# Performance work log

Hardware: AMD Instinct MI355X
Metric: run time of the kernel (lower is better)

Reference implementation:

```python
import jax, jax.numpy as jnp
import numpy as np

HEADS = 4

def setup_inputs() -> dict:
    B, L, D = 4, 2048, 256
    key = jax.random.key(0)
    k1, k2, k3, k4, k5, k6 = jax.random.split(key, 6)
    return {
        "atten": jax.random.normal(k1, (B, L, L), dtype=jnp.float32),
        "value": jax.random.normal(k2, (B, L, D), dtype=jnp.float32),
        "mask": jax.random.uniform(k3, (B, 1, L, L), dtype=jnp.float32),
        "padding_mask": jax.random.randint(k4, (B, L, L), 0, 2, dtype=jnp.int32),
        "Wv": jax.random.normal(k5, (D, D), dtype=jnp.float32) * 0.02,
        "bv": jnp.zeros((D,), dtype=jnp.float32),
        "Wo": jax.random.normal(k6, (D, D), dtype=jnp.float32) * 0.02,
        "bo": jnp.zeros((D,), dtype=jnp.float32),
    }

def reference(atten, value, mask, padding_mask, Wv, bv, Wo, bo):
    B, L, D = value.shape
    H = HEADS
    dk = D // H
    # to_value: Linear then split heads. N == 1 (value.unsqueeze(1) in torch).
    v = value @ Wv + bv                                   # (B, L, D)
    v = v.reshape(B, 1, L, H, dk).transpose(0, 3, 1, 2, 4)  # (B, H, N=1, L, dk)
    # externally supplied attention logits, two sequential masked fills
    a = atten[:, None, :, :]                              # (B, 1, L, L)
    a = jnp.where(mask < 0.5, jnp.finfo(a.dtype).min, a)
    a = jnp.where(padding_mask[:, None, :, :] == 0, -jnp.inf, a)
    a = jax.nn.softmax(a, axis=-1)                        # (B, 1, L, L)
    # dropout is identity in eval mode
    # einsum 'bhij,bhnjk->bhnik' with h=1 on a broadcast across H heads of v
    out = jnp.einsum('bij,bhnjk->bhnik', a[:, 0], v)      # (B, H, 1, L, dk)
    out = out.transpose(0, 2, 3, 1, 4).reshape(B, 1, L, D)
    out = out @ Wo + bo                                   # (B, 1, L, D)
    return out
```

## Files before the change

### kernel.cpp

```cpp
#include <hip/hip_runtime.h>
#include <hip/hip_bf16.h>
#include <math.h>

#define L 2048
#define D 256

typedef __attribute__((ext_vector_type(8))) short bf16x8;
typedef __attribute__((ext_vector_type(4))) float f32x4;
typedef __attribute__((ext_vector_type(4))) int i32x4;

__device__ __forceinline__ unsigned short f2bf(float f) {
    union { float f; unsigned int u; } v; v.f = f;
    unsigned int r = v.u + 0x7FFFu + ((v.u >> 16) & 1u);
    return (unsigned short)(r >> 16);
}

__global__ __launch_bounds__(256) void wtrans_kernel(
    const float* __restrict__ Wv, const float* __restrict__ Wo,
    unsigned short* __restrict__ Wvt, unsigned short* __restrict__ Wot) {
    int idx = blockIdx.x * 256 + threadIdx.x;
    int which = idx >> 16;
    int e = idx & 65535;
    int n = e >> 8, k = e & 255;
    const float* W = which ? Wo : Wv;
    unsigned short* Wt = which ? Wot : Wvt;
    Wt[n * 256 + k] = f2bf(W[k * 256 + n]);
}

__global__ __launch_bounds__(256) void gemm_v_kernel(
    const float* __restrict__ A,
    const unsigned short* __restrict__ Wt,
    const float* __restrict__ bias,
    unsigned short* __restrict__ Vt) {
    const int wave = threadIdx.x >> 6;
    const int lane = threadIdx.x & 63;
    const int mh = wave >> 1, nh = wave & 1;
    const int lm = lane & 15, q = lane >> 4;
    const int m0 = blockIdx.x * 64;
    const int n0 = blockIdx.y * 128;

    f32x4 acc[2][4];
#pragma unroll
    for (int i = 0; i < 2; i++)
#pragma unroll
        for (int j = 0; j < 4; j++) acc[i][j] = (f32x4)(0.f);

    int arow[2];
    arow[0] = m0 + mh * 32 + lm;
    arow[1] = arow[0] + 16;
    int ncol[4];
#pragma unroll
    for (int nf = 0; nf < 4; nf++) ncol[nf] = n0 + nh * 64 + nf * 16 + lm;

    for (int k0 = 0; k0 < 256; k0 += 32) {
        int kq = k0 + q * 8;
        bf16x8 bfr[4];
#pragma unroll
        for (int nf = 0; nf < 4; nf++)
            bfr[nf] = *reinterpret_cast<const bf16x8*>(Wt + ncol[nf] * 256 + kq);
        bf16x8 afr[2];
#pragma unroll
        for (int mf = 0; mf < 2; mf++) {
            const float* ap = A + arow[mf] * 256 + kq;
            f32x4 a0 = *reinterpret_cast<const f32x4*>(ap);
            f32x4 a1 = *reinterpret_cast<const f32x4*>(ap + 4);
            bf16x8 t;
#pragma unroll
            for (int e = 0; e < 4; e++) t[e] = (short)f2bf(a0[e]);
#pragma unroll
            for (int e = 0; e < 4; e++) t[4 + e] = (short)f2bf(a1[e]);
            afr[mf] = t;
        }
#pragma unroll
        for (int mf = 0; mf < 2; mf++)
#pragma unroll
            for (int nf = 0; nf < 4; nf++)
                acc[mf][nf] = __builtin_amdgcn_mfma_f32_16x16x32_bf16(
                    afr[mf], bfr[nf], acc[mf][nf], 0, 0, 0);
    }

#pragma unroll
    for (int mf = 0; mf < 2; mf++) {
        int mrow = m0 + mh * 32 + mf * 16 + q * 4;
#pragma unroll
        for (int nf = 0; nf < 4; nf++) {
            int n = ncol[nf];
            float bias_n = bias[n];
            int b = mrow >> 11;
            int j = mrow & 2047;
            unsigned short* dst = Vt + (size_t)b * (D * L) + (size_t)n * L + j;
            ushort4 pk;
            pk.x = f2bf(acc[mf][nf][0] + bias_n);
            pk.y = f2bf(acc[mf][nf][1] + bias_n);
            pk.z = f2bf(acc[mf][nf][2] + bias_n);
            pk.w = f2bf(acc[mf][nf][3] + bias_n);
            *reinterpret_cast<ushort4*>(dst) = pk;
        }
    }
}

__global__ __launch_bounds__(256) void p_kernel(
    const float* __restrict__ atten, const float* __restrict__ mask,
    const int* __restrict__ pad, unsigned short* __restrict__ P,
    float* __restrict__ lsum2) {
    const int wid = blockIdx.x * 4 + (threadIdx.x >> 6);
    const int row = wid >> 1, h = wid & 1;
    const int lane = threadIdx.x & 63;

    const size_t base = (size_t)row * L + h * 1024 + lane * 4;
    const float* at = atten + base;
    const float* mk = mask  + base;
    const int*   pd = pad   + base;
    unsigned short* Pr = P + base;

    f32x4 a0 = *reinterpret_cast<const f32x4*>(at);
    f32x4 m0 = *reinterpret_cast<const f32x4*>(mk);
    i32x4 p0 = *reinterpret_cast<const i32x4*>(pd);

    float l_th = 0.f;
#pragma unroll
    for (int c = 0; c < 4; c++) {
        f32x4 a1, m1; i32x4 p1;
        if (c < 3) {
            const int off = (c + 1) * 256;
            a1 = *reinterpret_cast<const f32x4*>(at + off);
            m1 = *reinterpret_cast<const f32x4*>(mk + off);
            p1 = *reinterpret_cast<const i32x4*>(pd + off);
        }
        ushort4 pk;
        float pv;
        pv = (m0[0] < 0.5f || p0[0] == 0) ? 0.f : __expf(a0[0]); l_th += pv; pk.x = f2bf(pv);
        pv = (m0[1] < 0.5f || p0[1] == 0) ? 0.f : __expf(a0[1]); l_th += pv; pk.y = f2bf(pv);
        pv = (m0[2] < 0.5f || p0[2] == 0) ? 0.f : __expf(a0[2]); l_th += pv; pk.z = f2bf(pv);
        pv = (m0[3] < 0.5f || p0[3] == 0) ? 0.f : __expf(a0[3]); l_th += pv; pk.w = f2bf(pv);
        *reinterpret_cast<ushort4*>(Pr + c * 256) = pk;
        a0 = a1; m0 = m1; p0 = p1;
    }
#pragma unroll
    for (int off = 1; off < 64; off <<= 1) l_th += __shfl_xor(l_th, off);
    if (lane == 0) lsum2[wid] = l_th;
}

__global__ __launch_bounds__(256) void pv_split_kernel(
    const unsigned short* __restrict__ P, const unsigned short* __restrict__ Vt,
    float* __restrict__ part) {
    const int rb = blockIdx.x;
    const int sk = blockIdx.y;
    const int tid = threadIdx.x;
    const int w = tid >> 6, lane = tid & 63;
    const int lm = lane & 15, q = lane >> 4;
    const int b = rb >> 6;
    const int row0 = rb * 32;

    const unsigned short* pA = P + (size_t)row0 * L + sk * 512 + q * 8;
    const unsigned short* pB = Vt + (size_t)b * (D * L) + (size_t)(w * 64) * L
                             + sk * 512 + q * 8;

    f32x4 acc[2][4];
#pragma unroll
    for (int i = 0; i < 2; i++)
#pragma unroll
        for (int j = 0; j < 4; j++) acc[i][j] = (f32x4)(0.f);

    bf16x8 Ac[2], Bc[4], An[2], Bn[4];
#pragma unroll
    for (int mf = 0; mf < 2; mf++)
        Ac[mf] = *reinterpret_cast<const bf16x8*>(pA + (mf * 16 + lm) * L);
#pragma unroll
    for (int nf = 0; nf < 4; nf++)
        Bc[nf] = *reinterpret_cast<const bf16x8*>(pB + (nf * 16 + lm) * L);

    for (int t = 0; t < 16; t++) {
        if (t < 15) {
            const int kn = (t + 1) * 32;
#pragma unroll
            for (int mf = 0; mf < 2; mf++)
                An[mf] = *reinterpret_cast<const bf16x8*>(pA + (mf * 16 + lm) * L + kn);
#pragma unroll
            for (int nf = 0; nf < 4; nf++)
                Bn[nf] = *reinterpret_cast<const bf16x8*>(pB + (nf * 16 + lm) * L + kn);
        }
#pragma unroll
        for (int mf = 0; mf < 2; mf++)
#pragma unroll
            for (int nf = 0; nf < 4; nf++)
                acc[mf][nf] = __builtin_amdgcn_mfma_f32_16x16x32_bf16(
                    Ac[mf], Bc[nf], acc[mf][nf], 0, 0, 0);
#pragma unroll
        for (int mf = 0; mf < 2; mf++) Ac[mf] = An[mf];
#pragma unroll
        for (int nf = 0; nf < 4; nf++) Bc[nf] = Bn[nf];
    }

    float* pb = part + ((size_t)sk * 256 + rb) * (32 * 256);
#pragma unroll
    for (int mf = 0; mf < 2; mf++)
#pragma unroll
        for (int nf = 0; nf < 4; nf++) {
            int col = w * 64 + nf * 16 + lm;
#pragma unroll
            for (int rg = 0; rg < 4; rg++)
                pb[(mf * 16 + q * 4 + rg) * 256 + col] = acc[mf][nf][rg];
        }
}

__global__ __launch_bounds__(256) void combine_gemm_kernel(
    const float* __restrict__ part, const float* __restrict__ lsum2,
    const unsigned short* __restrict__ Wot, const float* __restrict__ bo,
    float* __restrict__ out) {
    const int cb = blockIdx.x;
    const int tid = threadIdx.x;
    const int w = tid >> 6, lane = tid & 63;
    const int lm = lane & 15, q = lane >> 4;
    const int rb = cb >> 1;
    const int rlo = (cb & 1) * 16;

    __shared__ __align__(16) unsigned short Alds[16][264];

    {
        const int r16 = tid >> 4;
        const int c0 = (tid & 15) * 16;
        const int g = cb * 16 + r16;
        float l = lsum2[2 * g] + lsum2[2 * g + 1];
        float inv = 1.f / l;
        const float* pb = part + (size_t)rb * (32 * 256) + (rlo + r16) * 256 + c0;
#pragma unroll
        for (int e = 0; e < 16; e += 4) {
            f32x4 s = (f32x4)(0.f);
#pragma unroll
            for (int skp = 0; skp < 4; skp++)
                s += *reinterpret_cast<const f32x4*>(pb + (size_t)skp * (256 * 32 * 256) + e);
            s *= inv;
            ushort4 pk;
            pk.x = f2bf(s[0]); pk.y = f2bf(s[1]); pk.z = f2bf(s[2]); pk.w = f2bf(s[3]);
            *reinterpret_cast<ushort4*>(&Alds[r16][c0 + e]) = pk;
        }
    }
    __syncthreads();

    f32x4 oacc[4];
#pragma unroll
    for (int j = 0; j < 4; j++) oacc[j] = (f32x4)(0.f);
    int ncol[4];
#pragma unroll
    for (int nf = 0; nf < 4; nf++) ncol[nf] = w * 64 + nf * 16 + lm;

    for (int kk = 0; kk < 8; kk++) {
        int kq = kk * 32 + q * 8;
        bf16x8 bfr[4];
#pragma unroll
        for (int nf = 0; nf < 4; nf++)
            bfr[nf] = *reinterpret_cast<const bf16x8*>(Wot + ncol[nf] * 256 + kq);
        bf16x8 afr = *reinterpret_cast<const bf16x8*>(&Alds[lm][kq]);
#pragma unroll
        for (int nf = 0; nf < 4; nf++)
            oacc[nf] = __builtin_amdgcn_mfma_f32_16x16x32_bf16(
                afr, bfr[nf], oacc[nf], 0, 0, 0);
    }

    const int mrow = cb * 16 + q * 4;
#pragma unroll
    for (int nf = 0; nf < 4; nf++) {
        int n = ncol[nf];
        float bn = bo[n];
#pragma unroll
        for (int rg = 0; rg < 4; rg++)
            out[(size_t)(mrow + rg) * 256 + n] = oacc[nf][rg] + bn;
    }
}

extern "C" void kernel_launch(void* const* d_in, const int* in_sizes, int n_in,
                              void* d_out, int out_size, void* d_ws, size_t ws_size,
                              hipStream_t stream) {
    (void)in_sizes; (void)n_in; (void)out_size; (void)ws_size;
    const float* atten = (const float*)d_in[0];
    const float* value = (const float*)d_in[1];
    const float* mask  = (const float*)d_in[2];
    const int*   pad   = (const int*)d_in[3];
    const float* Wv    = (const float*)d_in[4];
    const float* bv    = (const float*)d_in[5];
    const float* Wo    = (const float*)d_in[6];
    const float* bo    = (const float*)d_in[7];
    float* out = (float*)d_out;

    char* ws = (char*)d_ws;
    unsigned short* Vt  = (unsigned short*)(ws);
    unsigned short* Wvt = (unsigned short*)(ws + 4194304);
    unsigned short* Wot = (unsigned short*)(ws + 4325376);
    unsigned short* P   = (unsigned short*)(ws + 4456448);
    float* lsum2        = (float*)(ws + 38010880);
    float* part         = (float*)(ws + 38076416);

    wtrans_kernel<<<512, 256, 0, stream>>>(Wv, Wo, Wvt, Wot);
    gemm_v_kernel<<<dim3(128, 2), 256, 0, stream>>>(value, Wvt, bv, Vt);
    p_kernel<<<4096, 256, 0, stream>>>(atten, mask, pad, P, lsum2);
    pv_split_kernel<<<dim3(256, 4), 256, 0, stream>>>(P, Vt, part);
    combine_gemm_kernel<<<512, 256, 0, stream>>>(part, lsum2, Wot, bo, out);
}
```

Baseline: 289.2 us.

## Fuse PV GEMM with normalization and output projection, drop split-K partials

Replaces the split-K PV kernel and separate combine/output-projection kernel with one kernel that accumulates the full K range for 16 rows, normalizes by the row sums, and applies Wo in shared memory. This removes the fp32 partial-sum write and read and one launch. It costs less row reuse of Vt per block and fewer, longer blocks. The softmax-numerator kernel also issues all its loads up front and gets an occupancy hint.

```diff
diff --git a/kernel.cpp b/kernel.cpp
--- a/kernel.cpp
+++ b/kernel.cpp
@@ -99,7 +99,7 @@
     }
 }
 
-__global__ __launch_bounds__(256) void p_kernel(
+__global__ __launch_bounds__(256, 4) void p_kernel(
     const float* __restrict__ atten, const float* __restrict__ mask,
     const int* __restrict__ pad, unsigned short* __restrict__ P,
     float* __restrict__ lsum2) {
@@ -113,128 +113,96 @@
     const int*   pd = pad   + base;
     unsigned short* Pr = P + base;
 
-    f32x4 a0 = *reinterpret_cast<const f32x4*>(at);
-    f32x4 m0 = *reinterpret_cast<const f32x4*>(mk);
-    i32x4 p0 = *reinterpret_cast<const i32x4*>(pd);
+    f32x4 a[4], m[4]; i32x4 p[4];
+#pragma unroll
+    for (int c = 0; c < 4; c++) a[c] = *reinterpret_cast<const f32x4*>(at + c * 256);
+#pragma unroll
+    for (int c = 0; c < 4; c++) m[c] = *reinterpret_cast<const f32x4*>(mk + c * 256);
+#pragma unroll
+    for (int c = 0; c < 4; c++) p[c] = *reinterpret_cast<const i32x4*>(pd + c * 256);
 
     float l_th = 0.f;
 #pragma unroll
     for (int c = 0; c < 4; c++) {
-        f32x4 a1, m1; i32x4 p1;
-        if (c < 3) {
-            const int off = (c + 1) * 256;
-            a1 = *reinterpret_cast<const f32x4*>(at + off);
-            m1 = *reinterpret_cast<const f32x4*>(mk + off);
-            p1 = *reinterpret_cast<const i32x4*>(pd + off);
-        }
         ushort4 pk;
         float pv;
-        pv = (m0[0] < 0.5f || p0[0] == 0) ? 0.f : __expf(a0[0]); l_th += pv; pk.x = f2bf(pv);
-        pv = (m0[1] < 0.5f || p0[1] == 0) ? 0.f : __expf(a0[1]); l_th += pv; pk.y = f2bf(pv);
-        pv = (m0[2] < 0.5f || p0[2] == 0) ? 0.f : __expf(a0[2]); l_th += pv; pk.z = f2bf(pv);
-        pv = (m0[3] < 0.5f || p0[3] == 0) ? 0.f : __expf(a0[3]); l_th += pv; pk.w = f2bf(pv);
+        pv = (m[c][0] < 0.5f || p[c][0] == 0) ? 0.f : __expf(a[c][0]); l_th += pv; pk.x = f2bf(pv);
+        pv = (m[c][1] < 0.5f || p[c][1] == 0) ? 0.f : __expf(a[c][1]); l_th += pv; pk.y = f2bf(pv);
+        pv = (m[c][2] < 0.5f || p[c][2] == 0) ? 0.f : __expf(a[c][2]); l_th += pv; pk.z = f2bf(pv);
+        pv = (m[c][3] < 0.5f || p[c][3] == 0) ? 0.f : __expf(a[c][3]); l_th += pv; pk.w = f2bf(pv);
         *reinterpret_cast<ushort4*>(Pr + c * 256) = pk;
-        a0 = a1; m0 = m1; p0 = p1;
     }
 #pragma unroll
     for (int off = 1; off < 64; off <<= 1) l_th += __shfl_xor(l_th, off);
     if (lane == 0) lsum2[wid] = l_th;
 }
 
-__global__ __launch_bounds__(256) void pv_split_kernel(
+__global__ __launch_bounds__(256, 2) void pv_out_kernel(
     const unsigned short* __restrict__ P, const unsigned short* __restrict__ Vt,
-    float* __restrict__ part) {
+    const float* __restrict__ lsum2, const unsigned short* __restrict__ Wot,
+    const float* __restrict__ bo, float* __restrict__ out) {
     const int rb = blockIdx.x;
-    const int sk = blockIdx.y;
     const int tid = threadIdx.x;
     const int w = tid >> 6, lane = tid & 63;
     const int lm = lane & 15, q = lane >> 4;
-    const int b = rb >> 6;
-    const int row0 = rb * 32;
-
-    const unsigned short* pA = P + (size_t)row0 * L + sk * 512 + q * 8;
-    const unsigned short* pB = Vt + (size_t)b * (D * L) + (size_t)(w * 64) * L
-                             + sk * 512 + q * 8;
-
-    f32x4 acc[2][4];
-#pragma unroll
-    for (int i = 0; i < 2; i++)
-#pragma unroll
-        for (int j = 0; j < 4; j++) acc[i][j] = (f32x4)(0.f);
-
-    bf16x8 Ac[2], Bc[4], An[2], Bn[4];
-#pragma unroll
-    for (int mf = 0; mf < 2; mf++)
-        Ac[mf] = *reinterpret_cast<const bf16x8*>(pA + (mf * 16 + lm) * L);
-#pragma unroll
-    for (int nf = 0; nf < 4; nf++)
-        Bc[nf] = *reinterpret_cast<const bf16x8*>(pB + (nf * 16 + lm) * L);
-
-    for (int t = 0; t < 16; t++) {
-        if (t < 15) {
-            const int kn = (t + 1) * 32;
-#pragma unroll
-            for (int mf = 0; mf < 2; mf++)
-                An[mf] = *reinterpret_cast<const bf16x8*>(pA + (mf * 16 + lm) * L + kn);
+    const int b = rb >> 7;
+    const int row0 = rb * 16;
+
+    const unsigned short* pA = P + (size_t)row0 * L + (size_t)lm * L + q * 8;
+    const unsigned short* pB = Vt + (size_t)b * (D * L) + (size_t)(w * 64) * L + q * 8;
+
+    f32x4 acc[4];
+#pragma unroll
+    for (int j = 0; j < 4; j++) acc[j] = (f32x4)(0.f);
+
+    bf16x8 Ac[2], Bc[2][4], An[2], Bn[2][4];
+#pragma unroll
+    for (int kk = 0; kk < 2; kk++) {
+        Ac[kk] = *reinterpret_cast<const bf16x8*>(pA + kk * 32);
+#pragma unroll
+        for (int nf = 0; nf < 4; nf++)
+            Bc[kk][nf] = *reinterpret_cast<const bf16x8*>(pB + (nf * 16 + lm) * L + kk * 32);
+    }
+
+    for (int t = 0; t < 32; t++) {
+        if (t < 31) {
+            const int kn = (t + 1) * 64;
+#pragma unroll
+            for (int kk = 0; kk < 2; kk++) {
+                An[kk] = *reinterpret_cast<const bf16x8*>(pA + kn + kk * 32);
+#pragma unroll
+                for (int nf = 0; nf < 4; nf++)
+                    Bn[kk][nf] = *reinterpret_cast<const bf16x8*>(
+                        pB + (nf * 16 + lm) * L + kn + kk * 32);
+            }
+        }
+#pragma unroll
+        for (int kk = 0; kk < 2; kk++)
 #pragma unroll
             for (int nf = 0; nf < 4; nf++)
-                Bn[nf] = *reinterpret_cast<const bf16x8*>(pB + (nf * 16 + lm) * L + kn);
-        }
-#pragma unroll
-        for (int mf = 0; mf < 2; mf++)
-#pragma unroll
-            for (int nf = 0; nf < 4; nf++)
-                acc[mf][nf] = __builtin_amdgcn_mfma_f32_16x16x32_bf16(
-                    Ac[mf], Bc[nf], acc[mf][nf], 0, 0, 0);
-#pragma unroll
-        for (int mf = 0; mf < 2; mf++) Ac[mf] = An[mf];
-#pragma unroll
-        for (int nf = 0; nf < 4; nf++) Bc[nf] = Bn[nf];
-    }
-
-    float* pb = part + ((size_t)sk * 256 + rb) * (32 * 256);
-#pragma unroll
-    for (int mf = 0; mf < 2; mf++)
-#pragma unroll
-        for (int nf = 0; nf < 4; nf++) {
-            int col = w * 64 + nf * 16 + lm;
-#pragma unroll
-            for (int rg = 0; rg < 4; rg++)
-                pb[(mf * 16 + q * 4 + rg) * 256 + col] = acc[mf][nf][rg];
-        }
-}
-
-__global__ __launch_bounds__(256) void combine_gemm_kernel(
-    const float* __restrict__ part, const float* __restrict__ lsum2,
-    const unsigned short* __restrict__ Wot, const float* __restrict__ bo,
-    float* __restrict__ out) {
-    const int cb = blockIdx.x;
-    const int tid = threadIdx.x;
-    const int w = tid >> 6, lane = tid & 63;
-    const int lm = lane & 15, q = lane >> 4;
-    const int rb = cb >> 1;
-    const int rlo = (cb & 1) * 16;
+                acc[nf] = __builtin_amdgcn_mfma_f32_16x16x32_bf16(
+                    Ac[kk], Bc[kk][nf], acc[nf], 0, 0, 0);
+#pragma unroll
+        for (int kk = 0; kk < 2; kk++) {
+            Ac[kk] = An[kk];
+#pragma unroll
+            for (int nf = 0; nf < 4; nf++) Bc[kk][nf] = Bn[kk][nf];
+        }
+    }
 
     __shared__ __align__(16) unsigned short Alds[16][264];
-
-    {
-        const int r16 = tid >> 4;
-        const int c0 = (tid & 15) * 16;
-        const int g = cb * 16 + r16;
-        float l = lsum2[2 * g] + lsum2[2 * g + 1];
-        float inv = 1.f / l;
-        const float* pb = part + (size_t)rb * (32 * 256) + (rlo + r16) * 256 + c0;
-#pragma unroll
-        for (int e = 0; e < 16; e += 4) {
-            f32x4 s = (f32x4)(0.f);
-#pragma unroll
-            for (int skp = 0; skp < 4; skp++)
-                s += *reinterpret_cast<const f32x4*>(pb + (size_t)skp * (256 * 32 * 256) + e);
-            s *= inv;
-            ushort4 pk;
-            pk.x = f2bf(s[0]); pk.y = f2bf(s[1]); pk.z = f2bf(s[2]); pk.w = f2bf(s[3]);
-            *reinterpret_cast<ushort4*>(&Alds[r16][c0 + e]) = pk;
-        }
+    float inv[4];
+#pragma unroll
+    for (int rg = 0; rg < 4; rg++) {
+        int gr = row0 + q * 4 + rg;
+        inv[rg] = 1.f / (lsum2[2 * gr] + lsum2[2 * gr + 1]);
+    }
+#pragma unroll
+    for (int nf = 0; nf < 4; nf++) {
+        int col = w * 64 + nf * 16 + lm;
+#pragma unroll
+        for (int rg = 0; rg < 4; rg++)
+            Alds[q * 4 + rg][col] = f2bf(acc[nf][rg] * inv[rg]);
     }
     __syncthreads();
 
@@ -258,7 +226,7 @@
                 afr, bfr[nf], oacc[nf], 0, 0, 0);
     }
 
-    const int mrow = cb * 16 + q * 4;
+    const int mrow = row0 + q * 4;
 #pragma unroll
     for (int nf = 0; nf < 4; nf++) {
         int n = ncol[nf];
@@ -289,11 +257,9 @@
     unsigned short* Wot = (unsigned short*)(ws + 4325376);
     unsigned short* P   = (unsigned short*)(ws + 4456448);
     float* lsum2        = (float*)(ws + 38010880);
-    float* part         = (float*)(ws + 38076416);
 
     wtrans_kernel<<<512, 256, 0, stream>>>(Wv, Wo, Wvt, Wot);
     gemm_v_kernel<<<dim3(128, 2), 256, 0, stream>>>(value, Wvt, bv, Vt);
     p_kernel<<<4096, 256, 0, stream>>>(atten, mask, pad, P, lsum2);
-    pv_split_kernel<<<dim3(256, 4), 256, 0, stream>>>(P, Vt, part);
-    combine_gemm_kernel<<<512, 256, 0, stream>>>(part, lsum2, Wot, bo, out);
-}
+    pv_out_kernel<<<512, 256, 0, stream>>>(P, Vt, lsum2, Wot, bo, out);
+}
```

New measurement: 304.7 us. 5.4% more time.
